# Optimization experiments

Hardware: AMD Instinct MI355X
Metric: run time of the kernel (lower is better)

The kernel has to match this reference:

```python
import jax, jax.numpy as jnp
import numpy as np

N, E, IN, H, G = 50000, 800000, 200, 128, 512
L, M = 2, 2
D = H - 1  # Lorentz space dims
EPS = 1e-5


def _l_inner(x, y):
    return -x[..., :1] * y[..., :1] + jnp.sum(x[..., 1:] * y[..., 1:], -1, keepdims=True)


def _proj(x, c):
    s = x[..., 1:]
    t = jnp.sqrt(c + jnp.sum(s * s, -1, keepdims=True))
    return jnp.concatenate([t, s], -1)


def _expmap0(v, c):
    u = v[..., 1:]
    n = jnp.maximum(jnp.linalg.norm(u, axis=-1, keepdims=True), 1e-9)
    sc = jnp.sqrt(c)
    return jnp.concatenate([sc * jnp.cosh(n / sc), sc * jnp.sinh(n / sc) * u / n], -1)


def _logmap0(x, c):
    y = x[..., 1:]
    yn = jnp.maximum(jnp.linalg.norm(y, axis=-1, keepdims=True), 1e-9)
    sc = jnp.sqrt(c)
    d = sc * jnp.arccosh(jnp.maximum(x[..., :1] / sc, 1.0 + EPS))
    return jnp.concatenate([jnp.zeros_like(d), d * y / yn], -1)


def _dist(x, y, c):
    inner = -x[..., 0] * y[..., 0] + jnp.sum(x[..., 1:] * y[..., 1:], -1)
    val = jnp.maximum(-inner / c, 1.0 + EPS)
    return jnp.sqrt(c) * jnp.arccosh(val)


def _hyp_linear(x, w, b, c):
    v = _logmap0(x, c)                      # [n, H], time comp = 0
    os = v[..., 1:] @ w.T + b               # [n, D]
    return _proj(_expmap0(jnp.concatenate([v[..., :1], os], -1), c), c)


def _hyp_act(x, c):
    v = _logmap0(x, c)
    vs = jnp.tanh(v[..., 1:])
    return _expmap0(jnp.concatenate([jnp.zeros_like(v[..., :1]), vs], -1), c)


def _centroid(att, x, src, dst, c):
    # sparse weighted sum: m[i] = sum_{(i,j) in E} att_ij * x[j], then Lorentz normalize
    m = jax.ops.segment_sum(att[:, None] * x[dst], src, num_segments=N)
    denom = jnp.sqrt(jnp.maximum(-_l_inner(m, m), 1e-9))
    return jnp.sqrt(c) * m / denom


def _gin_layer(h, src, dst, aw, ab, eps, mw, mb, c):
    # distance-based attention on linearly transformed features
    hl = _hyp_linear(h, aw, ab, c)
    att = jnp.exp(-_dist(hl[src], hl[dst], c))   # [E]
    agg = _proj(_centroid(att, h, src, dst, c), c)
    hp = _proj(h, c)
    v = _logmap0(agg, c) + (1.0 + eps) * _logmap0(hp, c)
    out = _proj(_expmap0(v, c), c)
    for m in range(M):
        out = _hyp_act(_hyp_linear(out, mw[m], mb[m], c), c)
    return out


def setup_inputs() -> dict:
    key = jax.random.key(0)
    ks = jax.random.split(key, 8)
    x = jax.random.normal(ks[0], (N, IN), jnp.float32) * 0.1
    w_in = jax.random.normal(ks[1], (IN, D), jnp.float32) * (1.0 / np.sqrt(IN))
    att_w = jax.random.normal(ks[2], (L, D, D), jnp.float32) * (1.0 / np.sqrt(D))
    att_b = jnp.zeros((L, D), jnp.float32)
    mlp_w = jax.random.normal(ks[3], (L, M, D, D), jnp.float32) * (1.0 / np.sqrt(D))
    mlp_b = jnp.zeros((L, M, D), jnp.float32)
    eps = jnp.full((L,), 0.1, jnp.float32)
    c = jnp.ones((1,), jnp.float32)
    edge_index = jax.random.randint(ks[4], (2, E), 0, N)
    batch = jnp.sort(jax.random.randint(ks[5], (N,), 0, G))
    return {"x": x, "c": c, "w_in": w_in, "att_w": att_w, "att_b": att_b,
            "eps": eps, "mlp_w": mlp_w, "mlp_b": mlp_b,
            "edge_index": edge_index, "batch": batch}


def reference(x, c, w_in, att_w, att_b, eps, mlp_w, mlp_b, edge_index, batch):
    cc = c[0]
    src, dst = edge_index[0], edge_index[1]
    # Euclidean input proj -> tangent vector at origin -> manifold
    v0 = jnp.concatenate([jnp.zeros((x.shape[0], 1), x.dtype), x @ w_in], -1)
    h = _proj(_expmap0(v0, cc), cc)
    pooled = []
    for l in range(L):
        h = _gin_layer(h, src, dst, att_w[l], att_b[l], eps[l], mlp_w[l], mlp_b[l], cc)
        pooled.append(jax.ops.segment_sum(_logmap0(h, cc), batch, num_segments=G))
    return jnp.concatenate(pooled, -1)  # [G, L*H]
```

## Files before the change

### kernel.cpp

```cpp
#include <hip/hip_runtime.h>
#include <hip/hip_fp16.h>
#include <math.h>

#define NN 50000
#define NNP 50048
#define EE 800000
#define IN_F 200
#define DD 127
#define GG 512
#define EPSH 1e-5f
#define PS_SCALE 0.015625f

typedef unsigned int u32;
typedef unsigned short u16;
typedef __attribute__((ext_vector_type(8))) short short8;
typedef __attribute__((ext_vector_type(4))) float f32x4;
typedef _Float16 h2f __attribute__((ext_vector_type(2)));
typedef __fp16 fp16x2 __attribute__((ext_vector_type(2)));
union UH {
  u32 u;
  h2f h;
  fp16x2 f;
};

__device__ __forceinline__ u32 bf16r(float x) {
  u32 u = __float_as_uint(x);
  return (u + 0x7fffu + ((u >> 16) & 1u)) >> 16;
}

__device__ __forceinline__ u32 packhl(float v) {
  u32 hi = bf16r(v);
  float vh = __uint_as_float(hi << 16);
  u32 lo = bf16r(v - vh);
  return hi | (lo << 16);
}

__device__ __forceinline__ float rec(u32 u) {
  return __uint_as_float(u << 16) + __uint_as_float(u & 0xffff0000u);
}

__device__ __forceinline__ u32 pk2h(float a, float b) {
#if __has_builtin(__builtin_amdgcn_cvt_pkrtz)
  UH x;
  x.f = __builtin_amdgcn_cvt_pkrtz(a, b);
  return x.u;
#else
  __half2 r = __floats2half2_rn(a, b);
  return *(u32*)&r;
#endif
}

__device__ __forceinline__ float fdot2h(u32 a, u32 b, float acc) {
  UH ua, ub;
  ua.u = a;
  ub.u = b;
#if __has_builtin(__builtin_amdgcn_fdot2)
  return __builtin_amdgcn_fdot2(ua.h, ub.h, acc, false);
#else
  acc = fmaf((float)ua.h[0], (float)ub.h[0], acc);
  return fmaf((float)ua.h[1], (float)ub.h[1], acc);
#endif
}

#define WF_TOT (28672 + 6 * 16384)
__global__ void k_prep_wf(const float* __restrict__ att_w, const float* __restrict__ mlp_w,
                          const float* __restrict__ w_in, u16* __restrict__ Wfh,
                          u16* __restrict__ Wfl) {
  for (int idx = blockIdx.x * 256 + threadIdx.x; idx < WF_TOT; idx += gridDim.x * 256) {
    float val;
    if (idx < 28672) {
      int q = idx >> 12, rem = idx & 4095;
      int t = rem >> 9, l = (rem >> 3) & 63, j = rem & 7;
      int k = q * 32 + ((l >> 4) << 3) + j, n = t * 16 + (l & 15);
      val = (k < IN_F && n < DD) ? w_in[k * DD + n] : 0.f;
    } else {
      int rel = idx - 28672;
      int mat = rel >> 14, rem = rel & 16383;
      int q = rem >> 12;
      rem &= 4095;
      int t = rem >> 9, l = (rem >> 3) & 63, j = rem & 7;
      int k = q * 32 + ((l >> 4) << 3) + j, n = t * 16 + (l & 15);
      const float* wsrc = (mat < 2) ? att_w + mat * DD * DD : mlp_w + (mat - 2) * DD * DD;
      val = (k < DD && n < DD) ? wsrc[n * DD + k] : 0.f;
    }
    u32 hi = bf16r(val);
    float vh = __uint_as_float(hi << 16);
    u32 lo = bf16r(val - vh);
    Wfh[idx] = (u16)hi;
    Wfl[idx] = (u16)lo;
  }
}

__global__ void k_count(const int* __restrict__ idx, int n, int* __restrict__ cnt) {
  int i = blockIdx.x * blockDim.x + threadIdx.x;
  if (i < n) atomicAdd(&cnt[idx[i]], 1);
}

__global__ __launch_bounds__(1024) void k_scan_excl(const int* __restrict__ in, int n,
                                                    int* __restrict__ out, int* __restrict__ cur) {
  __shared__ int wbase[16];
  __shared__ int chunk_tot;
  int tid = threadIdx.x;
  int lane = tid & 63;
  int w = tid >> 6;
  int carry = 0;
  for (int base = 0; base < n; base += 4096) {
    int i0 = base + tid * 4;
    int v[4];
#pragma unroll
    for (int j = 0; j < 4; j++) v[j] = (i0 + j < n) ? in[i0 + j] : 0;
    int x = v[0] + v[1] + v[2] + v[3];
    int incl = x;
#pragma unroll
    for (int off = 1; off < 64; off <<= 1) {
      int t = __shfl_up(incl, off);
      if (lane >= off) incl += t;
    }
    if (lane == 63) wbase[w] = incl;
    __syncthreads();
    if (w == 0) {
      int t = (lane < 16) ? wbase[lane] : 0;
      int it = t;
#pragma unroll
      for (int off = 1; off < 16; off <<= 1) {
        int v2 = __shfl_up(it, off);
        if (lane >= off) it += v2;
      }
      if (lane < 16) wbase[lane] = it - t;
      if (lane == 15) chunk_tot = it;
    }
    __syncthreads();
    int run = carry + wbase[w] + (incl - x);
#pragma unroll
    for (int j = 0; j < 4; j++) {
      if (i0 + j < n) {
        out[i0 + j] = run;
        if (cur) cur[i0 + j] = run;
      }
      run += v[j];
    }
    carry += chunk_tot;
    __syncthreads();
  }
  if (tid == 0) out[n] = carry;
}

__global__ void k_scatter(const int* __restrict__ src, const int* __restrict__ dst, int n,
                          int* __restrict__ cursor, int* __restrict__ dst_sorted) {
  int e = blockIdx.x * blockDim.x + threadIdx.x;
  if (e < n) {
    int s = src[e];
    int slot = atomicAdd(&cursor[s], 1);
    dst_sorted[slot] = dst[e];
  }
}

__global__ void k_gptr(const int* __restrict__ batch, int* __restrict__ gptr) {
  int g = blockIdx.x * blockDim.x + threadIdx.x;
  if (g > GG) return;
  int lo = 0, hi = NN;
  while (lo < hi) {
    int mid = (lo + hi) >> 1;
    if (batch[mid] < g) lo = mid + 1; else hi = mid;
  }
  gptr[g] = lo;
}

union AB {
  short8 v;
  u32 w[4];
};

__device__ __forceinline__ void build_hl(const float* xv, AB& ah, AB& al) {
#pragma unroll
  for (int p = 0; p < 4; p++) {
    u32 h0 = bf16r(xv[2 * p]), h1 = bf16r(xv[2 * p + 1]);
    float f0 = __uint_as_float(h0 << 16), f1 = __uint_as_float(h1 << 16);
    ah.w[p] = h0 | (h1 << 16);
    al.w[p] = bf16r(xv[2 * p] - f0) | (bf16r(xv[2 * p + 1] - f1) << 16);
  }
}

__device__ __forceinline__ void mfma3(const AB& ah, const AB& al, const u16* __restrict__ Wh,
                                      const u16* __restrict__ Wl, int q, int lane, f32x4* acc) {
  const u16* bph = Wh + ((size_t)(q * 8) * 64 + lane) * 8;
  const u16* bpl = Wl + ((size_t)(q * 8) * 64 + lane) * 8;
#pragma unroll
  for (int t = 0; t < 8; t++) {
    short8 bh = *(const short8*)(bph + t * 512);
    short8 bl = *(const short8*)(bpl + t * 512);
    acc[t] = __builtin_amdgcn_mfma_f32_16x16x32_bf16(ah.v, bh, acc[t], 0, 0, 0);
    acc[t] = __builtin_amdgcn_mfma_f32_16x16x32_bf16(al.v, bh, acc[t], 0, 0, 0);
    acc[t] = __builtin_amdgcn_mfma_f32_16x16x32_bf16(ah.v, bl, acc[t], 0, 0, 0);
  }
}

__device__ __forceinline__ void gemm_packhl(const u32* __restrict__ A32, int mld,
                                            const u16* __restrict__ Wh,
                                            const u16* __restrict__ Wl, int lane, int quad,
                                            f32x4* acc) {
#pragma unroll
  for (int q = 0; q < 4; q++) {
    int k0 = q * 32 + quad * 8;
    const u32* ap = A32 + (size_t)mld * 128 + k0;
    uint4 u0 = *(const uint4*)ap;
    uint4 u1 = *(const uint4*)(ap + 4);
    u32 uu[8] = {u0.x, u0.y, u0.z, u0.w, u1.x, u1.y, u1.z, u1.w};
    AB ah, al;
#pragma unroll
    for (int p = 0; p < 4; p++) {
      ah.w[p] = __builtin_amdgcn_perm(uu[2 * p + 1], uu[2 * p], 0x05040100u);
      al.w[p] = __builtin_amdgcn_perm(uu[2 * p + 1], uu[2 * p], 0x07060302u);
    }
    mfma3(ah, al, Wh, Wl, q, lane, acc);
  }
}

__device__ __forceinline__ void gemm_lds(const float (*tile)[129], int ml, int quad, int lane,
                                         const u16* __restrict__ Wh, const u16* __restrict__ Wl,
                                         f32x4* acc) {
#pragma unroll
  for (int q = 0; q < 4; q++) {
    int k0 = q * 32 + quad * 8;
    float xv[8];
#pragma unroll
    for (int j = 0; j < 8; j++) xv[j] = tile[ml][k0 + j];
    AB ah, al;
    build_hl(xv, ah, al);
    mfma3(ah, al, Wh, Wl, q, lane, acc);
  }
}

__device__ __forceinline__ void bias8(const float* __restrict__ bias, int ml, float* bj) {
#pragma unroll
  for (int t = 0; t < 8; t++) {
    int col = t * 16 + ml;
    bj[t] = (bias != nullptr && col < DD) ? bias[col] : 0.f;
  }
}

template <int TANH>
__device__ __forceinline__ void row_vs(const f32x4* acc, const float* bj, int r, float* vs) {
#pragma unroll
  for (int t = 0; t < 8; t++) {
    float v = acc[t][r] + bj[t];
    if (TANH) {
      float e = exp2f(v * 2.8853900817779268f);
      v = 1.f - 2.f / (e + 1.f);
    }
    vs[t] = v;
  }
}

__device__ __forceinline__ void store_T_row(const float* vs, u32* __restrict__ To, int rowD,
                                            int ml) {
  u32* to = To + (size_t)rowD * 128 + ml;
#pragma unroll
  for (int t = 0; t < 8; t++) to[t * 16] = packhl(vs[t]);
}

__device__ __forceinline__ void store_P_row(const float* vs, u32* __restrict__ Pb,
                                            float* __restrict__ Pt, int rowD, int ml, float cc,
                                            float sc, float pscale) {
  float ps = 0.f;
#pragma unroll
  for (int t = 0; t < 8; t++) ps += vs[t] * vs[t];
#pragma unroll
  for (int off = 1; off < 16; off <<= 1) ps += __shfl_xor(ps, off);
  float nn = fmaxf(sqrtf(ps), 1e-9f);
  float e = expf(nn / sc);
  float f = sc * (e - 1.f / e) * 0.5f / nn;
  float tt = sqrtf(cc + f * f * ps);
  f *= pscale;
  u32* pb = Pb + (size_t)rowD * 128 + ml;
#pragma unroll
  for (int t = 0; t < 4; t++) pb[t * 16] = pk2h(f * vs[t], f * vs[t + 4]);
  if (ml == 0) Pt[rowD * 2] = pscale * tt;
}

__global__ __launch_bounds__(256) void k_gemm_in(
    const float* __restrict__ x, const u16* __restrict__ WhI, const u16* __restrict__ WlI,
    const u16* __restrict__ WhA, const u16* __restrict__ WlA, const float* __restrict__ attb,
    u32* __restrict__ To, u32* __restrict__ HHh, float* __restrict__ ptF,
    const float* __restrict__ cptr, int M) {
  __shared__ float tile[4][16][129];
  int lane = threadIdx.x & 63, wid = threadIdx.x >> 6;
  int m0 = blockIdx.x * 64 + wid * 16;
  int ml = lane & 15, quad = lane >> 4;
  int mld = m0 + ml;
  f32x4 acc[8];
#pragma unroll
  for (int t = 0; t < 8; t++) acc[t] = (f32x4){0.f, 0.f, 0.f, 0.f};
#pragma unroll
  for (int q = 0; q < 7; q++) {
    int k0 = q * 32 + quad * 8;
    bool ok = (mld < M) && (k0 + 7 < IN_F);
    const float* ap = x + (size_t)mld * IN_F + k0;
    float4 x0 = ok ? *(const float4*)ap : make_float4(0.f, 0.f, 0.f, 0.f);
    float4 x1 = ok ? *(const float4*)(ap + 4) : make_float4(0.f, 0.f, 0.f, 0.f);
    float xv[8] = {x0.x, x0.y, x0.z, x0.w, x1.x, x1.y, x1.z, x1.w};
    AB ah, al;
    build_hl(xv, ah, al);
    mfma3(ah, al, WhI, WlI, q, lane, acc);
  }
  float cc = *cptr, sc = sqrtf(cc);
  {
    float bj[8];
    bias8(nullptr, ml, bj);
#pragma unroll
    for (int r = 0; r < 4; r++) {
      int rowD = m0 + quad * 4 + r;
      float vs[8];
      row_vs<0>(acc, bj, r, vs);
      if (rowD < M) {
        store_T_row(vs, To, rowD, ml);
        store_P_row(vs, HHh + 64, ptF + 1, rowD, ml, cc, sc, PS_SCALE);
      }
#pragma unroll
      for (int t = 0; t < 8; t++) tile[wid][quad * 4 + r][t * 16 + ml] = vs[t];
    }
  }
#pragma unroll
  for (int t = 0; t < 8; t++) acc[t] = (f32x4){0.f, 0.f, 0.f, 0.f};
  gemm_lds(tile[wid], ml, quad, lane, WhA, WlA, acc);
  {
    float bj[8];
    bias8(attb, ml, bj);
#pragma unroll
    for (int r = 0; r < 4; r++) {
      int rowD = m0 + quad * 4 + r;
      float vs[8];
      row_vs<0>(acc, bj, r, vs);
      if (rowD < M) store_P_row(vs, HHh, ptF, rowD, ml, cc, sc, 1.f);
    }
  }
}

template <int LAST>
__global__ __launch_bounds__(256) void k_mlp3(
    const u32* __restrict__ A32, const u16* __restrict__ Wha, const u16* __restrict__ Wla,
    const float* __restrict__ ba, const u16* __restrict__ Whb, const u16* __restrict__ Wlb,
    const float* __restrict__ bb, const u16* __restrict__ WhA, const u16* __restrict__ WlA,
    const float* __restrict__ attb, u32* __restrict__ To, u32* __restrict__ HHh,
    float* __restrict__ ptF, const float* __restrict__ cptr, int M) {
  __shared__ float tile[4][16][129];
  int lane = threadIdx.x & 63, wid = threadIdx.x >> 6;
  int m0 = blockIdx.x * 64 + wid * 16;
  int ml = lane & 15, quad = lane >> 4;
  int mld = m0 + ml;
  f32x4 acc[8];
#pragma unroll
  for (int t = 0; t < 8; t++) acc[t] = (f32x4){0.f, 0.f, 0.f, 0.f};
  gemm_packhl(A32, mld, Wha, Wla, lane, quad, acc);
  {
    float bj[8];
    bias8(ba, ml, bj);
#pragma unroll
    for (int r = 0; r < 4; r++) {
      float vs[8];
      row_vs<1>(acc, bj, r, vs);
#pragma unroll
      for (int t = 0; t < 8; t++) tile[wid][quad * 4 + r][t * 16 + ml] = vs[t];
    }
  }
#pragma unroll
  for (int t = 0; t < 8; t++) acc[t] = (f32x4){0.f, 0.f, 0.f, 0.f};
  gemm_lds(tile[wid], ml, quad, lane, Whb, Wlb, acc);
  float cc = 1.f, sc = 1.f;
  if (!LAST) {
    cc = *cptr;
    sc = sqrtf(cc);
  }
  {
    float bj[8];
    bias8(bb, ml, bj);
#pragma unroll
    for (int r = 0; r < 4; r++) {
      int rowD = m0 + quad * 4 + r;
      float vs[8];
      row_vs<1>(acc, bj, r, vs);
      if (rowD < M) store_T_row(vs, To, rowD, ml);
      if (!LAST) {
        if (rowD < M) store_P_row(vs, HHh + 64, ptF + 1, rowD, ml, cc, sc, PS_SCALE);
#pragma unroll
        for (int t = 0; t < 8; t++) tile[wid][quad * 4 + r][t * 16 + ml] = vs[t];
      }
    }
  }
  if (!LAST) {
#pragma unroll
    for (int t = 0; t < 8; t++) acc[t] = (f32x4){0.f, 0.f, 0.f, 0.f};
    gemm_lds(tile[wid], ml, quad, lane, WhA, WlA, acc);
    float bj[8];
    bias8(attb, ml, bj);
#pragma unroll
    for (int r = 0; r < 4; r++) {
      int rowD = m0 + quad * 4 + r;
      float vs[8];
      row_vs<0>(acc, bj, r, vs);
      if (rowD < M) store_P_row(vs, HHh, ptF, rowD, ml, cc, sc, 1.f);
    }
  }
}

__global__ __launch_bounds__(256) void k_agg_o(const u32* __restrict__ HHh,
                                               const float2* __restrict__ ptHH,
                                               const u32* __restrict__ T,
                                               const int* __restrict__ rowp,
                                               const int* __restrict__ dsts,
                                               const float* __restrict__ epsp,
                                               const float* __restrict__ cptr,
                                               u32* __restrict__ Tout, int n) {
  int node = blockIdx.x * 4 + (threadIdx.x >> 6);
  int lane = threadIdx.x & 63;
  if (node >= n) return;
  int o = lane & 7, g = lane >> 3;
  float c = *cptr, sc = sqrtf(c), rcpc = 1.f / c;
  float eps = *epsp;
  const u32* arow = HHh + (size_t)node * 128 + o * 8;
  uint4 a0 = *(const uint4*)arow;
  uint4 a1 = *(const uint4*)(arow + 4);
  u32 apk[8] = {a0.x, a0.y, a0.z, a0.w, a1.x, a1.y, a1.z, a1.w};
  float pts = ptHH[node].x;
  int e0 = rowp[node], e1 = rowp[node + 1];
  int iters = (e1 - e0 + 7) >> 3;
  h2f mpk[8];
  {
    UH z;
    z.u = 0;
#pragma unroll
    for (int j = 0; j < 8; j++) mpk[j] = z.h;
  }
  float mt = 0.f;
#pragma unroll 2
  for (int it = 0; it < iters; it++) {
    int e = e0 + it * 8 + g;
    bool ve = e < e1;
    int d = dsts[ve ? e : e0];
    const u32* rb = HHh + (size_t)d * 128 + o * 8;
    uint4 b0 = *(const uint4*)rb;
    uint4 b1 = *(const uint4*)(rb + 4);
    uint4 h0 = *(const uint4*)(rb + 64);
    uint4 h1 = *(const uint4*)(rb + 68);
    float2 pp = ptHH[d];
    u32 bw[8] = {b0.x, b0.y, b0.z, b0.w, b1.x, b1.y, b1.z, b1.w};
    float dot = 0.f;
#pragma unroll
    for (int j = 0; j < 8; j++) dot = fdot2h(apk[j], bw[j], dot);
    dot += __shfl_xor(dot, 1);
    dot += __shfl_xor(dot, 2);
    dot += __shfl_xor(dot, 4);
    float valv = fmaxf((pts * pp.x - dot) * rcpc, 1.f + EPSH);
    float w = valv + sqrtf(fmaf(valv, valv, -1.f));
    float att = exp2f(-sc * __log2f(w));
    att = ve ? att : 0.f;
    UH att2;
    att2.u = pk2h(att, att);
    u32 hw[8] = {h0.x, h0.y, h0.z, h0.w, h1.x, h1.y, h1.z, h1.w};
#pragma unroll
    for (int j = 0; j < 8; j++) {
      UH hv;
      hv.u = hw[j];
      mpk[j] = att2.h * hv.h + mpk[j];
    }
    mt = fmaf(att, pp.y, mt);
  }
#pragma unroll
  for (int off = 8; off <= 32; off <<= 1) {
#pragma unroll
    for (int j = 0; j < 8; j++) {
      UH v;
      v.h = mpk[j];
      UH s;
      s.u = (u32)__shfl_xor((int)v.u, off);
      mpk[j] = v.h + s.h;
    }
    mt += __shfl_xor(mt, off);
  }
  float lp = 0.f;
#pragma unroll
  for (int j = 0; j < 8; j++) {
    float lo = (float)mpk[j][0], hi = (float)mpk[j][1];
    lp = fmaf(lo, lo, lp);
    lp = fmaf(hi, hi, lp);
  }
  lp += __shfl_xor(lp, 1);
  lp += __shfl_xor(lp, 2);
  lp += __shfl_xor(lp, 4);
  float lsq = lp;
  float neg_inner = mt * mt - lsq;
  float denom = sqrtf(fmaxf(neg_inner, 1e-9f));
  float r = sc / denom;
  float ssq = r * r * lsq;
  float agg0 = sqrtf(c + ssq);
  float ynA = fmaxf(sqrtf(ssq), 1e-9f);
  float v2 = fmaxf(agg0 / sc, 1.f + EPSH);
  float dA = sc * 0.69314718056f * __log2f(v2 + sqrtf(v2 * v2 - 1.f));
  float sca = dA * r / ynA;
  if (g == 0) {
    const u32* tp = T + (size_t)node * 128 + o * 8;
    uint4 t0 = *(const uint4*)tp;
    uint4 t0b = *(const uint4*)(tp + 4);
    uint4 t1 = *(const uint4*)(tp + 64);
    uint4 t1b = *(const uint4*)(tp + 68);
    u32 tw[8] = {t0.x, t0.y, t0.z, t0.w, t0b.x, t0b.y, t0b.z, t0b.w};
    u32 tv[8] = {t1.x, t1.y, t1.z, t1.w, t1b.x, t1b.y, t1b.z, t1b.w};
    float oe = 1.f + eps;
    u32 olo[8], ohi[8];
#pragma unroll
    for (int j = 0; j < 8; j++) {
      float lo = (float)mpk[j][0], hi = (float)mpk[j][1];
      olo[j] = packhl(fmaf(sca, lo, oe * rec(tw[j])));
      ohi[j] = packhl(fmaf(sca, hi, oe * rec(tv[j])));
    }
    u32* op = Tout + (size_t)node * 128 + o * 8;
    *(uint4*)op = make_uint4(olo[0], olo[1], olo[2], olo[3]);
    *(uint4*)(op + 4) = make_uint4(olo[4], olo[5], olo[6], olo[7]);
    *(uint4*)(op + 64) = make_uint4(ohi[0], ohi[1], ohi[2], ohi[3]);
    *(uint4*)(op + 68) = make_uint4(ohi[4], ohi[5], ohi[6], ohi[7]);
  }
}

__global__ void k_pool(const u32* __restrict__ U, const int* __restrict__ gptr,
                       float* __restrict__ out, int layer) {
  int g = blockIdx.x;
  int c = threadIdx.x;
  int s = gptr[g], e = gptr[g + 1];
  float acc = 0.f;
  if (c > 0) {
    const u32* up = U + (c - 1);
    int i = s;
    float a0 = 0.f, a1 = 0.f, a2 = 0.f, a3 = 0.f;
    for (; i + 3 < e; i += 4) {
      a0 += rec(up[(size_t)i * 128]);
      a1 += rec(up[(size_t)(i + 1) * 128]);
      a2 += rec(up[(size_t)(i + 2) * 128]);
      a3 += rec(up[(size_t)(i + 3) * 128]);
    }
    for (; i < e; i++) a0 += rec(up[(size_t)i * 128]);
    acc = (a0 + a1) + (a2 + a3);
  }
  out[(size_t)g * 256 + layer * 128 + c] = acc;
}

extern "C" void kernel_launch(void* const* d_in, const int* in_sizes, int n_in, void* d_out,
                              int out_size, void* d_ws, size_t ws_size, hipStream_t stream) {
  const float* x = (const float*)d_in[0];
  const float* cptr = (const float*)d_in[1];
  const float* w_in = (const float*)d_in[2];
  const float* att_w = (const float*)d_in[3];
  const float* att_b = (const float*)d_in[4];
  const float* epsv = (const float*)d_in[5];
  const float* mlp_w = (const float*)d_in[6];
  const float* mlp_b = (const float*)d_in[7];
  const int* ei = (const int*)d_in[8];
  const int* batch = (const int*)d_in[9];
  const int* srcp = ei;
  const int* dstp = ei + EE;
  float* out = (float*)d_out;

  u32* ws = (u32*)d_ws;
  u16* Wfh = (u16*)ws;
  u16* Wfl = Wfh + WF_TOT;
  int* deg = (int*)(ws + 126976);
  int* rowp = deg + NN;
  int* cursor = rowp + NN + 1;
  int* gptr = cursor + NN;
  int* dsts = gptr + GG + 1;
  size_t o1 = (size_t)((u32*)(dsts + EE) - ws);
  o1 = (o1 + 3) & ~(size_t)3;
  float2* ptHH = (float2*)(ws + o1);
  u32* HHh = ws + o1 + 2 * NNP;
  u32* A32 = HHh + (size_t)NNP * 128;
  u32* B32 = A32 + (size_t)NNP * 128;

  const int EW = 12500;
  const int GEMMG = (NN + 63) / 64;
  float* ptF = (float*)ptHH;

  (void)hipMemsetAsync(deg, 0, NN * sizeof(int), stream);
  k_prep_wf<<<64, 256, 0, stream>>>(att_w, mlp_w, w_in, Wfh, Wfl);
  k_count<<<(EE + 255) / 256, 256, 0, stream>>>(srcp, EE, deg);
  k_gptr<<<3, 256, 0, stream>>>(batch, gptr);
  k_scan_excl<<<1, 1024, 0, stream>>>(deg, NN, rowp, cursor);
  k_scatter<<<(EE + 255) / 256, 256, 0, stream>>>(srcp, dstp, EE, cursor, dsts);

#define WH(m) (Wfh + 28672 + (m) * 16384)
#define WL(m) (Wfl + 28672 + (m) * 16384)

  k_gemm_in<<<GEMMG, 256, 0, stream>>>(x, Wfh, Wfl, WH(0), WL(0), att_b, A32, HHh, ptF, cptr, NN);

  k_agg_o<<<EW, 256, 0, stream>>>(HHh, ptHH, A32, rowp, dsts, epsv + 0, cptr, B32, NN);
  k_mlp3<0><<<GEMMG, 256, 0, stream>>>(B32, WH(2), WL(2), mlp_b + 0 * DD, WH(3), WL(3),
                                       mlp_b + 1 * DD, WH(1), WL(1), att_b + DD, A32, HHh, ptF,
                                       cptr, NN);
  k_pool<<<GG, 128, 0, stream>>>(A32, gptr, out, 0);

  k_agg_o<<<EW, 256, 0, stream>>>(HHh, ptHH, A32, rowp, dsts, epsv + 1, cptr, B32, NN);
  k_mlp3<1><<<GEMMG, 256, 0, stream>>>(B32, WH(4), WL(4), mlp_b + 2 * DD, WH(5), WL(5),
                                       mlp_b + 3 * DD, nullptr, nullptr, nullptr, B32, nullptr,
                                       nullptr, cptr, NN);
  k_pool<<<GG, 128, 0, stream>>>(B32, gptr, out, 1);
}
```

Measured before the change: 522.1 us.

## Merge setup kernels, add c==1 attention fast path, spread aggregation epilogue across lanes

Three setup kernels (weight prep, gptr binary search, degree counting) are merged into one launch with block-range dispatch, which removes launch gaps. In the aggregation kernel, when sqrt(c)==1 the attention exp(-arccosh) is computed as a reciprocal of w instead of log2/exp2. The final output write is also spread across all 64 lanes instead of only the g==0 group: each lane selects one packed pair and writes scalar words, trading wide stores for more lanes doing work.

```diff
diff --git a/kernel.cpp b/kernel.cpp
--- a/kernel.cpp
+++ b/kernel.cpp
@@ -62,38 +62,61 @@
 #endif
 }
 
+__device__ __forceinline__ float frcp(float x) {
+#if __has_builtin(__builtin_amdgcn_rcpf)
+  return __builtin_amdgcn_rcpf(x);
+#else
+  return 1.f / x;
+#endif
+}
+
 #define WF_TOT (28672 + 6 * 16384)
-__global__ void k_prep_wf(const float* __restrict__ att_w, const float* __restrict__ mlp_w,
-                          const float* __restrict__ w_in, u16* __restrict__ Wfh,
-                          u16* __restrict__ Wfl) {
-  for (int idx = blockIdx.x * 256 + threadIdx.x; idx < WF_TOT; idx += gridDim.x * 256) {
-    float val;
-    if (idx < 28672) {
-      int q = idx >> 12, rem = idx & 4095;
-      int t = rem >> 9, l = (rem >> 3) & 63, j = rem & 7;
-      int k = q * 32 + ((l >> 4) << 3) + j, n = t * 16 + (l & 15);
-      val = (k < IN_F && n < DD) ? w_in[k * DD + n] : 0.f;
-    } else {
-      int rel = idx - 28672;
-      int mat = rel >> 14, rem = rel & 16383;
-      int q = rem >> 12;
-      rem &= 4095;
-      int t = rem >> 9, l = (rem >> 3) & 63, j = rem & 7;
-      int k = q * 32 + ((l >> 4) << 3) + j, n = t * 16 + (l & 15);
-      const float* wsrc = (mat < 2) ? att_w + mat * DD * DD : mlp_w + (mat - 2) * DD * DD;
-      val = (k < DD && n < DD) ? wsrc[n * DD + k] : 0.f;
-    }
-    u32 hi = bf16r(val);
-    float vh = __uint_as_float(hi << 16);
-    u32 lo = bf16r(val - vh);
-    Wfh[idx] = (u16)hi;
-    Wfl[idx] = (u16)lo;
-  }
-}
-
-__global__ void k_count(const int* __restrict__ idx, int n, int* __restrict__ cnt) {
-  int i = blockIdx.x * blockDim.x + threadIdx.x;
-  if (i < n) atomicAdd(&cnt[idx[i]], 1);
+#define SETUP_PREP_BLKS 64
+#define SETUP_GPTR_BLKS 3
+__global__ void k_setup(const float* __restrict__ att_w, const float* __restrict__ mlp_w,
+                        const float* __restrict__ w_in, u16* __restrict__ Wfh,
+                        u16* __restrict__ Wfl, const int* __restrict__ batch,
+                        int* __restrict__ gptr, const int* __restrict__ srcp,
+                        int* __restrict__ deg) {
+  int b = blockIdx.x, tid = threadIdx.x;
+  if (b < SETUP_PREP_BLKS) {
+    for (int idx = b * 256 + tid; idx < WF_TOT; idx += SETUP_PREP_BLKS * 256) {
+      float val;
+      if (idx < 28672) {
+        int q = idx >> 12, rem = idx & 4095;
+        int t = rem >> 9, l = (rem >> 3) & 63, j = rem & 7;
+        int k = q * 32 + ((l >> 4) << 3) + j, n = t * 16 + (l & 15);
+        val = (k < IN_F && n < DD) ? w_in[k * DD + n] : 0.f;
+      } else {
+        int rel = idx - 28672;
+        int mat = rel >> 14, rem = rel & 16383;
+        int q = rem >> 12;
+        rem &= 4095;
+        int t = rem >> 9, l = (rem >> 3) & 63, j = rem & 7;
+        int k = q * 32 + ((l >> 4) << 3) + j, n = t * 16 + (l & 15);
+        const float* wsrc = (mat < 2) ? att_w + mat * DD * DD : mlp_w + (mat - 2) * DD * DD;
+        val = (k < DD && n < DD) ? wsrc[n * DD + k] : 0.f;
+      }
+      u32 hi = bf16r(val);
+      float vh = __uint_as_float(hi << 16);
+      u32 lo = bf16r(val - vh);
+      Wfh[idx] = (u16)hi;
+      Wfl[idx] = (u16)lo;
+    }
+  } else if (b < SETUP_PREP_BLKS + SETUP_GPTR_BLKS) {
+    int g = (b - SETUP_PREP_BLKS) * 256 + tid;
+    if (g <= GG) {
+      int lo = 0, hi = NN;
+      while (lo < hi) {
+        int mid = (lo + hi) >> 1;
+        if (batch[mid] < g) lo = mid + 1; else hi = mid;
+      }
+      gptr[g] = lo;
+    }
+  } else {
+    int i = (b - SETUP_PREP_BLKS - SETUP_GPTR_BLKS) * 256 + tid;
+    if (i < EE) atomicAdd(&deg[srcp[i]], 1);
+  }
 }
 
 __global__ __launch_bounds__(1024) void k_scan_excl(const int* __restrict__ in, int n,
@@ -153,17 +176,6 @@
     int slot = atomicAdd(&cursor[s], 1);
     dst_sorted[slot] = dst[e];
   }
-}
-
-__global__ void k_gptr(const int* __restrict__ batch, int* __restrict__ gptr) {
-  int g = blockIdx.x * blockDim.x + threadIdx.x;
-  if (g > GG) return;
-  int lo = 0, hi = NN;
-  while (lo < hi) {
-    int mid = (lo + hi) >> 1;
-    if (batch[mid] < g) lo = mid + 1; else hi = mid;
-  }
-  gptr[g] = lo;
 }
 
 union AB {
@@ -416,6 +428,7 @@
   if (node >= n) return;
   int o = lane & 7, g = lane >> 3;
   float c = *cptr, sc = sqrtf(c), rcpc = 1.f / c;
+  bool sc1 = (sc == 1.0f);
   float eps = *epsp;
   const u32* arow = HHh + (size_t)node * 128 + o * 8;
   uint4 a0 = *(const uint4*)arow;
@@ -452,7 +465,11 @@
     dot += __shfl_xor(dot, 4);
     float valv = fmaxf((pts * pp.x - dot) * rcpc, 1.f + EPSH);
     float w = valv + sqrtf(fmaf(valv, valv, -1.f));
-    float att = exp2f(-sc * __log2f(w));
+    float att;
+    if (sc1)
+      att = frcp(w);
+    else
+      att = exp2f(-sc * __log2f(w));
     att = ve ? att : 0.f;
     UH att2;
     att2.u = pk2h(att, att);
@@ -497,28 +514,22 @@
   float v2 = fmaxf(agg0 / sc, 1.f + EPSH);
   float dA = sc * 0.69314718056f * __log2f(v2 + sqrtf(v2 * v2 - 1.f));
   float sca = dA * r / ynA;
-  if (g == 0) {
-    const u32* tp = T + (size_t)node * 128 + o * 8;
-    uint4 t0 = *(const uint4*)tp;
-    uint4 t0b = *(const uint4*)(tp + 4);
-    uint4 t1 = *(const uint4*)(tp + 64);
-    uint4 t1b = *(const uint4*)(tp + 68);
-    u32 tw[8] = {t0.x, t0.y, t0.z, t0.w, t0b.x, t0b.y, t0b.z, t0b.w};
-    u32 tv[8] = {t1.x, t1.y, t1.z, t1.w, t1b.x, t1b.y, t1b.z, t1b.w};
-    float oe = 1.f + eps;
-    u32 olo[8], ohi[8];
-#pragma unroll
-    for (int j = 0; j < 8; j++) {
-      float lo = (float)mpk[j][0], hi = (float)mpk[j][1];
-      olo[j] = packhl(fmaf(sca, lo, oe * rec(tw[j])));
-      ohi[j] = packhl(fmaf(sca, hi, oe * rec(tv[j])));
-    }
-    u32* op = Tout + (size_t)node * 128 + o * 8;
-    *(uint4*)op = make_uint4(olo[0], olo[1], olo[2], olo[3]);
-    *(uint4*)(op + 4) = make_uint4(olo[4], olo[5], olo[6], olo[7]);
-    *(uint4*)(op + 64) = make_uint4(ohi[0], ohi[1], ohi[2], ohi[3]);
-    *(uint4*)(op + 68) = make_uint4(ohi[4], ohi[5], ohi[6], ohi[7]);
-  }
+  int s = o * 8 + g;
+  u32 msel = 0;
+#pragma unroll
+  for (int j = 0; j < 8; j++) {
+    UH v;
+    v.h = mpk[j];
+    if (j == g) msel = v.u;
+  }
+  UH mm;
+  mm.u = msel;
+  float mlo = (float)mm.h[0], mhi = (float)mm.h[1];
+  float oe = 1.f + eps;
+  u32 t0 = T[(size_t)node * 128 + s];
+  u32 t1 = T[(size_t)node * 128 + 64 + s];
+  Tout[(size_t)node * 128 + s] = packhl(fmaf(sca, mlo, oe * rec(t0)));
+  Tout[(size_t)node * 128 + 64 + s] = packhl(fmaf(sca, mhi, oe * rec(t1)));
 }
 
 __global__ void k_pool(const u32* __restrict__ U, const int* __restrict__ gptr,
@@ -576,12 +587,11 @@
 
   const int EW = 12500;
   const int GEMMG = (NN + 63) / 64;
+  const int SETUPG = SETUP_PREP_BLKS + SETUP_GPTR_BLKS + (EE + 255) / 256;
   float* ptF = (float*)ptHH;
 
   (void)hipMemsetAsync(deg, 0, NN * sizeof(int), stream);
-  k_prep_wf<<<64, 256, 0, stream>>>(att_w, mlp_w, w_in, Wfh, Wfl);
-  k_count<<<(EE + 255) / 256, 256, 0, stream>>>(srcp, EE, deg);
-  k_gptr<<<3, 256, 0, stream>>>(batch, gptr);
+  k_setup<<<SETUPG, 256, 0, stream>>>(att_w, mlp_w, w_in, Wfh, Wfl, batch, gptr, srcp, deg);
   k_scan_excl<<<1, 1024, 0, stream>>>(deg, NN, rowp, cursor);
   k_scatter<<<(EE + 255) / 256, 256, 0, stream>>>(srcp, dstp, EE, cursor, dsts);
 
```

Measured after the change: 508.5 us. -2.6%, faster.
